# Optimization experiments

Measured on AMD Instinct MI355X. Metric: run time of the kernel, lower is better.

The kernel has to match this reference:

```python
import jax, jax.numpy as jnp
import numpy as np

B, S, D, H = 2, 2048, 1024, 16
DK = D // H
SCALE = DK ** 0.5


def setup_inputs() -> dict:
    key = jax.random.key(0)
    ks = jax.random.split(key, 5)
    std = 1.0 / np.sqrt(D)
    return {
        "x": jax.random.normal(ks[0], (B, S, D), dtype=jnp.float32),
        "Wq": jax.random.normal(ks[1], (D, D), dtype=jnp.float32) * std,
        "Wk": jax.random.normal(ks[2], (D, D), dtype=jnp.float32) * std,
        "Wv": jax.random.normal(ks[3], (D, D), dtype=jnp.float32) * std,
        "Wo": jax.random.normal(ks[4], (D, D), dtype=jnp.float32) * std,
    }


def _split_heads(t):
    # [B, S, D] -> [B, H, S, DK]
    b, s, d = t.shape
    return t.reshape(b, s, H, DK).transpose(0, 2, 1, 3)


def reference(x, Wq, Wk, Wv, Wo):
    b, s, d = x.shape
    q = _split_heads(x @ Wq)
    k = _split_heads(x @ Wk)
    v = _split_heads(x @ Wv)
    # scores: [B, H, S, S]
    score = jnp.einsum("bhqd,bhkd->bhqk", q, k)
    causal = jnp.tril(jnp.ones((s, s), dtype=bool))[None, None]
    score = jnp.where(causal, score, -jnp.inf)
    attn = jax.nn.softmax(score / SCALE, axis=-1)
    out = jnp.einsum("bhqk,bhkd->bhqd", attn, v)
    out = out.transpose(0, 2, 1, 3).reshape(b, s, d)
    return out @ Wo
```

## Files before the change

### kernel.cpp

```cpp
#include <hip/hip_runtime.h>
#include <hip/hip_bf16.h>

typedef __bf16 bf16;
typedef __bf16 bf16x4 __attribute__((ext_vector_type(4)));
typedef __bf16 bf16x8 __attribute__((ext_vector_type(8)));
typedef float f32x4 __attribute__((ext_vector_type(4)));

#define MFMA16(a, b, c) __builtin_amdgcn_mfma_f32_16x16x32_bf16((a), (b), (c), 0, 0, 0)

__device__ __forceinline__ void async16(const void* g, void* l) {
  typedef const unsigned int __attribute__((address_space(1))) * GP;
  typedef unsigned int __attribute__((address_space(3))) * LP;
  __builtin_amdgcn_global_load_lds((GP)g, (LP)l, 16, 0, 0);
}

__global__ __launch_bounds__(256) void prep(
    const float* __restrict__ w0, const float* __restrict__ w1,
    const float* __restrict__ w2, const float* __restrict__ w3,
    const float* __restrict__ x, bf16* __restrict__ wtOut,
    bf16* __restrict__ xOut) {
  const int t = threadIdx.x;
  if (blockIdx.z == 4) {
    size_t base = ((size_t)(blockIdx.y * 16 + blockIdx.x)) * 16384;
#pragma unroll
    for (int p = 0; p < 16; ++p) {
      size_t i = base + (size_t)(p * 256 + t) * 4;
      f32x4 v = *(const f32x4*)&x[i];
      bf16 o[4];
#pragma unroll
      for (int j = 0; j < 4; ++j) o[j] = (bf16)v[j];
      *(ulong1*)&xOut[i] = *(ulong1*)o;
    }
    return;
  }
  __shared__ __align__(16) float tile[64][68];
  const float* src = (blockIdx.z == 0) ? w0 : (blockIdx.z == 1) ? w1
                   : (blockIdx.z == 2) ? w2 : w3;
  bf16* dst = wtOut + (size_t)blockIdx.z * (1024u * 1024u);
  const int bx = blockIdx.x, by = blockIdx.y;
#pragma unroll
  for (int p = 0; p < 4; ++p) {
    int idx = t + p * 256;
    int r = idx >> 4, c4 = idx & 15;
    *(f32x4*)&tile[r][c4 * 4] =
        *(const f32x4*)&src[(size_t)(by * 64 + r) * 1024 + bx * 64 + c4 * 4];
  }
  __syncthreads();
#pragma unroll
  for (int p = 0; p < 2; ++p) {
    int idx = t + p * 256;
    int rn = idx >> 3, c8 = idx & 7;
    bf16x8 v;
#pragma unroll
    for (int i = 0; i < 8; ++i) v[i] = (bf16)tile[c8 * 8 + i][rn];
    *(bf16x8*)&dst[(size_t)(bx * 64 + rn) * 1024 + by * 64 + c8 * 8] = v;
  }
}

template <typename OutT, int NI>
__global__ __launch_bounds__(256, 4) void gemm_bt(
    const bf16* __restrict__ A, const bf16* __restrict__ Bt,
    OutT* __restrict__ C, int btStrideZ, int cStrideZ, float scaleZ0,
    bf16* __restrict__ vtOut) {
  constexpr int XT = 1024 / (NI * 32);
  const int bid = blockIdx.x;
  const int rr = bid & 7, tt = bid >> 3;
  const int xb = tt % XT, yb = (tt / XT) * 8 + rr;
  const int zi = blockIdx.y;

  const int tid = threadIdx.x;
  const int wave = tid >> 6, lane = tid & 63;
  const int quad = lane >> 4, l16 = lane & 15;
  const int wm = wave >> 1, wn = wave & 1;
  const int m0 = yb * 128, n0 = xb * (NI * 32);
  const bf16* Bz = Bt + (size_t)zi * (size_t)btStrideZ;
  OutT* Cz = C + (size_t)zi * (size_t)cStrideZ;
  const float sc = (zi == 0) ? scaleZ0 : 1.0f;

  __shared__ __align__(16) bf16 lsA[2][128 * 32];
  __shared__ __align__(16) bf16 lsB[2][NI * 32 * 32];

  const int lrow = lane >> 2;
  const int cgX = (lane & 3) ^ ((lrow >> 1) & 3);
  const int fR = (l16 >> 1) & 3;

  f32x4 acc[4][NI];
#pragma unroll
  for (int i = 0; i < 4; ++i)
#pragma unroll
    for (int j = 0; j < NI; ++j) acc[i][j] = (f32x4){0.f, 0.f, 0.f, 0.f};

#pragma unroll
  for (int c = 0; c < 2; ++c) {
    int chunk = wave * 2 + c;
    int row = chunk * 16 + lrow;
    async16(&A[(size_t)(m0 + row) * 1024 + cgX * 8], &lsA[0][chunk * 512]);
  }
#pragma unroll
  for (int c = 0; c < NI / 2; ++c) {
    int chunk = wave * (NI / 2) + c;
    int row = chunk * 16 + lrow;
    async16(&Bz[(size_t)(n0 + row) * 1024 + cgX * 8], &lsB[0][chunk * 512]);
  }
  __syncthreads();

  for (int it = 0; it < 32; ++it) {
    const int cur = it & 1;
    if (it < 31) {
      int k0n = (it + 1) * 32;
#pragma unroll
      for (int c = 0; c < 2; ++c) {
        int chunk = wave * 2 + c;
        int row = chunk * 16 + lrow;
        async16(&A[(size_t)(m0 + row) * 1024 + k0n + cgX * 8],
                &lsA[cur ^ 1][chunk * 512]);
      }
#pragma unroll
      for (int c = 0; c < NI / 2; ++c) {
        int chunk = wave * (NI / 2) + c;
        int row = chunk * 16 + lrow;
        async16(&Bz[(size_t)(n0 + row) * 1024 + k0n + cgX * 8],
                &lsB[cur ^ 1][chunk * 512]);
      }
    }

    bf16x8 af[4], bfr[NI];
#pragma unroll
    for (int i = 0; i < 4; ++i) {
      int ra = wm * 64 + i * 16 + l16;
      af[i] = *(const bf16x8*)&lsA[cur][ra * 32 + ((quad ^ fR) * 8)];
    }
#pragma unroll
    for (int ni = 0; ni < NI; ++ni) {
      int rb = wn * (NI * 16) + ni * 16 + l16;
      bfr[ni] = *(const bf16x8*)&lsB[cur][rb * 32 + ((quad ^ fR) * 8)];
    }
#pragma unroll
    for (int mi = 0; mi < 4; ++mi)
#pragma unroll
      for (int ni = 0; ni < NI; ++ni)
        acc[mi][ni] = MFMA16(af[mi], bfr[ni], acc[mi][ni]);

    __syncthreads();
  }

  if (zi == 2 && vtOut != nullptr) {
#pragma unroll
    for (int mi = 0; mi < 4; ++mi)
#pragma unroll
      for (int ni = 0; ni < NI; ++ni) {
        int col = n0 + wn * (NI * 16) + ni * 16 + l16;
        int hd = col >> 6, d = col & 63;
        int row = m0 + wm * 64 + mi * 16 + quad * 4;
        int b = row >> 11, s = row & 2047;
        int s32 = s & 31;
        int sp = (s & ~31) + ((s32 & 12) << 1) + ((s32 >> 4) << 2);
        bf16 o[4];
#pragma unroll
        for (int r = 0; r < 4; ++r) o[r] = (bf16)acc[mi][ni][r];
        *(ulong1*)&vtOut[((size_t)(b * 16 + hd) * 64 + d) * 2048 + sp] =
            *(ulong1*)o;
      }
  } else {
#pragma unroll
    for (int mi = 0; mi < 4; ++mi)
#pragma unroll
      for (int ni = 0; ni < NI; ++ni) {
        int col = n0 + wn * (NI * 16) + ni * 16 + l16;
#pragma unroll
        for (int r = 0; r < 4; ++r) {
          int row = m0 + wm * 64 + mi * 16 + quad * 4 + r;
          Cz[(size_t)row * 1024 + col] = (OutT)(acc[mi][ni][r] * sc);
        }
      }
  }
}

__global__ __launch_bounds__(512, 4) void attn_fwd(
    const bf16* __restrict__ Q, const bf16* __restrict__ K,
    const bf16* __restrict__ Vt, bf16* __restrict__ O) {
  const int bid = blockIdx.x;
  const int x = bid & 15, hb = bid >> 4;
  const int h = hb & 15, b = hb >> 4;
  const int qt = b ? (15 - x) : x;
  const int tid = threadIdx.x;
  const int wave = tid >> 6, lane = tid & 63;
  const int quad = lane >> 4, l16 = lane & 15;

  __shared__ __align__(16) bf16 SMEM[16384];
  const int kof[2] = {0, 8192};
  const int vof[2] = {4096, 12288};
  bf16* Qs = &SMEM[8192];

  const size_t base = ((size_t)b * 2048) * 1024 + (size_t)h * 64;
  const bf16* Qb = Q + base;
  const bf16* Kb = K + base;
  const bf16* Vtb = Vt + ((size_t)(b * 16 + h)) * 64 * 2048;
  bf16* Ob = O + base;

  const int lrow = lane >> 3;
  const int cgX = (lane & 7) ^ lrow;

#pragma unroll
  for (int c = 0; c < 2; ++c) {
    int chunk = wave * 2 + c;
    int row = chunk * 8 + lrow;
    async16(&Qb[(size_t)(qt * 128 + row) * 1024 + cgX * 8], &Qs[chunk * 512]);
  }
  {
    int row = wave * 8 + lrow;
    async16(&Kb[(size_t)row * 1024 + cgX * 8], &SMEM[kof[0] + wave * 512]);
    async16(&Vtb[(size_t)row * 2048 + cgX * 8], &SMEM[vof[0] + wave * 512]);
  }
  __syncthreads();

  bf16x8 aq[2];
#pragma unroll
  for (int ks = 0; ks < 2; ++ks) {
    int row = wave * 16 + l16;
    aq[ks] = *(const bf16x8*)&Qs[row * 64 + (((ks * 4 + quad) ^ (l16 & 7)) * 8)];
  }
  __syncthreads();

  const float NEG_INF = -__builtin_inff();
  f32x4 lsv = (f32x4){0.f, 0.f, 0.f, 0.f};
  f32x4 Oacc[4];
#pragma unroll
  for (int nt = 0; nt < 4; ++nt) Oacc[nt] = (f32x4){0.f, 0.f, 0.f, 0.f};

  const int kt_end = 2 * qt + 1;
  const int ktd = 2 * qt + (wave >> 2);

  for (int kt = 0; kt <= kt_end; ++kt) {
    const int cur = kt & 1;
    if (kt < kt_end) {
      int row = wave * 8 + lrow;
      async16(&Kb[(size_t)((kt + 1) * 64 + row) * 1024 + cgX * 8],
              &SMEM[kof[cur ^ 1] + wave * 512]);
      async16(&Vtb[(size_t)row * 2048 + (kt + 1) * 64 + cgX * 8],
              &SMEM[vof[cur ^ 1] + wave * 512]);
    }

    if (kt <= ktd) {
      f32x4 sv[4];
#pragma unroll
      for (int nt = 0; nt < 4; ++nt) {
        int row = nt * 16 + l16;
        bf16x8 bk0 = *(const bf16x8*)&SMEM[kof[cur] + row * 64 +
                                           ((quad ^ (l16 & 7)) * 8)];
        bf16x8 bk1 = *(const bf16x8*)&SMEM[kof[cur] + row * 64 +
                                           (((4 + quad) ^ (l16 & 7)) * 8)];
        sv[nt] = (f32x4){0.f, 0.f, 0.f, 0.f};
        sv[nt] = MFMA16(bk0, aq[0], sv[nt]);
        sv[nt] = MFMA16(bk1, aq[1], sv[nt]);
      }

      if (kt == ktd) {
        const int q_rel = wave * 16 + l16;
        const int cb = (kt - 2 * qt) * 64;
#pragma unroll
        for (int nt = 0; nt < 4; ++nt) {
          const int kb = cb + nt * 16 + quad * 4;
#pragma unroll
          for (int r = 0; r < 4; ++r)
            if (kb + r > q_rel) sv[nt][r] = NEG_INF;
        }
      }

#pragma unroll
      for (int nt = 0; nt < 4; ++nt) {
#pragma unroll
        for (int r = 0; r < 4; ++r) sv[nt][r] = exp2f(sv[nt][r]);
        lsv += sv[nt];
      }
      bf16x8 apf[2];
#pragma unroll
      for (int a = 0; a < 2; ++a) {
        bf16x4 c0 = __builtin_convertvector(sv[2 * a], bf16x4);
        bf16x4 c1 = __builtin_convertvector(sv[2 * a + 1], bf16x4);
#pragma unroll
        for (int i = 0; i < 4; ++i) {
          apf[a][i] = c0[i];
          apf[a][4 + i] = c1[i];
        }
      }

#pragma unroll
      for (int nt = 0; nt < 4; ++nt) {
        const int R = nt * 16 + l16;
#pragma unroll
        for (int a = 0; a < 2; ++a) {
          bf16x8 bvf = *(const bf16x8*)&SMEM[vof[cur] + R * 64 +
                                             (((a * 4 + quad) ^ (l16 & 7)) *
                                              8)];
          Oacc[nt] = MFMA16(apf[a], bvf, Oacc[nt]);
        }
      }
    }

    __syncthreads();
  }

  float ls_acc = lsv[0] + lsv[1] + lsv[2] + lsv[3];
  ls_acc += __shfl_xor(ls_acc, 16, 64);
  ls_acc += __shfl_xor(ls_acc, 32, 64);
  float rl[4];
#pragma unroll
  for (int r = 0; r < 4; ++r) rl[r] = 1.f / __shfl(ls_acc, quad * 4 + r, 64);
#pragma unroll
  for (int nt = 0; nt < 4; ++nt)
#pragma unroll
    for (int r = 0; r < 4; ++r) {
      int row = qt * 128 + wave * 16 + quad * 4 + r;
      Ob[(size_t)row * 1024 + nt * 16 + l16] = (bf16)(Oacc[nt][r] * rl[r]);
    }
}

extern "C" void kernel_launch(void* const* d_in, const int* in_sizes, int n_in,
                              void* d_out, int out_size, void* d_ws,
                              size_t ws_size, hipStream_t stream) {
  (void)in_sizes; (void)n_in; (void)out_size; (void)ws_size;
  const float* x  = (const float*)d_in[0];
  const float* Wq = (const float*)d_in[1];
  const float* Wk = (const float*)d_in[2];
  const float* Wv = (const float*)d_in[3];
  const float* Wo = (const float*)d_in[4];
  float* out = (float*)d_out;

  bf16* ws = (bf16*)d_ws;
  const size_t WELEM = 1024u * 1024u;
  const size_t TELEM = 4096u * 1024u;
  bf16* wt  = ws;
  bf16* xbf = ws + 4 * WELEM;
  bf16* q   = xbf + TELEM;
  bf16* k   = q + TELEM;
  bf16* vt  = k + TELEM;
  bf16* ao  = vt + TELEM;

  const float QSCALE = 0.125f * 1.44269504088896340736f;

  prep<<<dim3(16, 16, 5), 256, 0, stream>>>(Wq, Wk, Wv, Wo, x, wt, xbf);
  gemm_bt<bf16, 4><<<dim3(256, 3), 256, 0, stream>>>(
      xbf, wt, q, (int)WELEM, (int)TELEM, QSCALE, vt);
  attn_fwd<<<dim3(512), 512, 0, stream>>>(q, k, vt, ao);
  gemm_bt<float, 2><<<dim3(512, 1), 256, 0, stream>>>(
      ao, wt + 3 * WELEM, out, 0, 0, 1.0f, nullptr);
}
```

Before: 171.1 us.

## Process KV tiles in pairs with four-slot LDS ring; enlarge output GEMM tile

The attention kernel now prefetches two K/V tiles ahead into a four-slot shared memory ring and handles two tiles per loop iteration, halving the number of block-wide barriers and deepening the prefetch. This doubles LDS use per block, which can lower how many blocks fit per CU. The final output projection GEMM switches to a larger tile variant with half as many blocks.

New measurement: 172.7 us. About the same (+1.0%).

```diff
diff --git a/kernel.cpp b/kernel.cpp
--- a/kernel.cpp
+++ b/kernel.cpp
@@ -187,10 +187,8 @@
   const int wave = tid >> 6, lane = tid & 63;
   const int quad = lane >> 4, l16 = lane & 15;
 
-  __shared__ __align__(16) bf16 SMEM[16384];
-  const int kof[2] = {0, 8192};
-  const int vof[2] = {4096, 12288};
-  bf16* Qs = &SMEM[8192];
+  __shared__ __align__(16) bf16 SMEM[32768];
+  bf16* Qs = &SMEM[16384];
 
   const size_t base = ((size_t)b * 2048) * 1024 + (size_t)h * 64;
   const bf16* Qb = Q + base;
@@ -209,8 +207,13 @@
   }
   {
     int row = wave * 8 + lrow;
-    async16(&Kb[(size_t)row * 1024 + cgX * 8], &SMEM[kof[0] + wave * 512]);
-    async16(&Vtb[(size_t)row * 2048 + cgX * 8], &SMEM[vof[0] + wave * 512]);
+    async16(&Kb[(size_t)row * 1024 + cgX * 8], &SMEM[0 * 8192 + wave * 512]);
+    async16(&Vtb[(size_t)row * 2048 + cgX * 8],
+            &SMEM[0 * 8192 + 4096 + wave * 512]);
+    async16(&Kb[(size_t)(64 + row) * 1024 + cgX * 8],
+            &SMEM[1 * 8192 + wave * 512]);
+    async16(&Vtb[(size_t)row * 2048 + 64 + cgX * 8],
+            &SMEM[1 * 8192 + 4096 + wave * 512]);
   }
   __syncthreads();
 
@@ -231,69 +234,84 @@
   const int kt_end = 2 * qt + 1;
   const int ktd = 2 * qt + (wave >> 2);
 
-  for (int kt = 0; kt <= kt_end; ++kt) {
-    const int cur = kt & 1;
-    if (kt < kt_end) {
+  for (int ktp = 0; ktp <= kt_end; ktp += 2) {
+    {
       int row = wave * 8 + lrow;
-      async16(&Kb[(size_t)((kt + 1) * 64 + row) * 1024 + cgX * 8],
-              &SMEM[kof[cur ^ 1] + wave * 512]);
-      async16(&Vtb[(size_t)row * 2048 + (kt + 1) * 64 + cgX * 8],
-              &SMEM[vof[cur ^ 1] + wave * 512]);
-    }
-
-    if (kt <= ktd) {
-      f32x4 sv[4];
-#pragma unroll
-      for (int nt = 0; nt < 4; ++nt) {
-        int row = nt * 16 + l16;
-        bf16x8 bk0 = *(const bf16x8*)&SMEM[kof[cur] + row * 64 +
-                                           ((quad ^ (l16 & 7)) * 8)];
-        bf16x8 bk1 = *(const bf16x8*)&SMEM[kof[cur] + row * 64 +
-                                           (((4 + quad) ^ (l16 & 7)) * 8)];
-        sv[nt] = (f32x4){0.f, 0.f, 0.f, 0.f};
-        sv[nt] = MFMA16(bk0, aq[0], sv[nt]);
-        sv[nt] = MFMA16(bk1, aq[1], sv[nt]);
-      }
-
-      if (kt == ktd) {
-        const int q_rel = wave * 16 + l16;
-        const int cb = (kt - 2 * qt) * 64;
+      if (ktp + 2 <= kt_end) {
+        int s2 = (ktp + 2) & 3;
+        async16(&Kb[(size_t)((ktp + 2) * 64 + row) * 1024 + cgX * 8],
+                &SMEM[s2 * 8192 + wave * 512]);
+        async16(&Vtb[(size_t)row * 2048 + (ktp + 2) * 64 + cgX * 8],
+                &SMEM[s2 * 8192 + 4096 + wave * 512]);
+      }
+      if (ktp + 3 <= kt_end) {
+        int s3 = (ktp + 3) & 3;
+        async16(&Kb[(size_t)((ktp + 3) * 64 + row) * 1024 + cgX * 8],
+                &SMEM[s3 * 8192 + wave * 512]);
+        async16(&Vtb[(size_t)row * 2048 + (ktp + 3) * 64 + cgX * 8],
+                &SMEM[s3 * 8192 + 4096 + wave * 512]);
+      }
+    }
+
+#pragma unroll
+    for (int sub = 0; sub < 2; ++sub) {
+      const int kt = ktp + sub;
+      const int ko = (kt & 3) * 8192;
+      const int vo = ko + 4096;
+      if (kt <= ktd) {
+        f32x4 sv[4];
 #pragma unroll
         for (int nt = 0; nt < 4; ++nt) {
-          const int kb = cb + nt * 16 + quad * 4;
-#pragma unroll
-          for (int r = 0; r < 4; ++r)
-            if (kb + r > q_rel) sv[nt][r] = NEG_INF;
-        }
-      }
-
-#pragma unroll
-      for (int nt = 0; nt < 4; ++nt) {
-#pragma unroll
-        for (int r = 0; r < 4; ++r) sv[nt][r] = exp2f(sv[nt][r]);
-        lsv += sv[nt];
-      }
-      bf16x8 apf[2];
-#pragma unroll
-      for (int a = 0; a < 2; ++a) {
-        bf16x4 c0 = __builtin_convertvector(sv[2 * a], bf16x4);
-        bf16x4 c1 = __builtin_convertvector(sv[2 * a + 1], bf16x4);
-#pragma unroll
-        for (int i = 0; i < 4; ++i) {
-          apf[a][i] = c0[i];
-          apf[a][4 + i] = c1[i];
-        }
-      }
-
-#pragma unroll
-      for (int nt = 0; nt < 4; ++nt) {
-        const int R = nt * 16 + l16;
+          int row = nt * 16 + l16;
+          bf16x8 bk0 = *(const bf16x8*)&SMEM[ko + row * 64 +
+                                             ((quad ^ (l16 & 7)) * 8)];
+          bf16x8 bk1 = *(const bf16x8*)&SMEM[ko + row * 64 +
+                                             (((4 + quad) ^ (l16 & 7)) * 8)];
+          sv[nt] = (f32x4){0.f, 0.f, 0.f, 0.f};
+          sv[nt] = MFMA16(bk0, aq[0], sv[nt]);
+          sv[nt] = MFMA16(bk1, aq[1], sv[nt]);
+        }
+
+        if (kt == ktd) {
+          const int q_rel = wave * 16 + l16;
+          const int cb = (kt - 2 * qt) * 64;
+#pragma unroll
+          for (int nt = 0; nt < 4; ++nt) {
+            const int kb = cb + nt * 16 + quad * 4;
+#pragma unroll
+            for (int r = 0; r < 4; ++r)
+              if (kb + r > q_rel) sv[nt][r] = NEG_INF;
+          }
+        }
+
+#pragma unroll
+        for (int nt = 0; nt < 4; ++nt) {
+#pragma unroll
+          for (int r = 0; r < 4; ++r) sv[nt][r] = exp2f(sv[nt][r]);
+          lsv += sv[nt];
+        }
+        bf16x8 apf[2];
 #pragma unroll
         for (int a = 0; a < 2; ++a) {
-          bf16x8 bvf = *(const bf16x8*)&SMEM[vof[cur] + R * 64 +
-                                             (((a * 4 + quad) ^ (l16 & 7)) *
-                                              8)];
-          Oacc[nt] = MFMA16(apf[a], bvf, Oacc[nt]);
+          bf16x4 c0 = __builtin_convertvector(sv[2 * a], bf16x4);
+          bf16x4 c1 = __builtin_convertvector(sv[2 * a + 1], bf16x4);
+#pragma unroll
+          for (int i = 0; i < 4; ++i) {
+            apf[a][i] = c0[i];
+            apf[a][4 + i] = c1[i];
+          }
+        }
+
+#pragma unroll
+        for (int nt = 0; nt < 4; ++nt) {
+          const int R = nt * 16 + l16;
+#pragma unroll
+          for (int a = 0; a < 2; ++a) {
+            bf16x8 bvf = *(const bf16x8*)&SMEM[vo + R * 64 +
+                                               (((a * 4 + quad) ^ (l16 & 7)) *
+                                                8)];
+            Oacc[nt] = MFMA16(apf[a], bvf, Oacc[nt]);
+          }
         }
       }
     }
@@ -343,6 +361,6 @@
   gemm_bt<bf16, 4><<<dim3(256, 3), 256, 0, stream>>>(
       xbf, wt, q, (int)WELEM, (int)TELEM, QSCALE, vt);
   attn_fwd<<<dim3(512), 512, 0, stream>>>(q, k, vt, ao);
-  gemm_bt<float, 2><<<dim3(512, 1), 256, 0, stream>>>(
+  gemm_bt<float, 4><<<dim3(256, 1), 256, 0, stream>>>(
       ao, wt + 3 * WELEM, out, 0, 0, 1.0f, nullptr);
 }
```
